# Performance work log

Hardware: AMD Instinct MI355X
Metric: run time of the kernel (lower is better)

## Reference

```python
import jax, jax.numpy as jnp
import numpy as np

H, CH, INF, EPS = 16, 24, 1e9, 1e-5

def layer_norm(x, w, b):
    mu = jnp.mean(x, axis=-1, keepdims=True)
    var = jnp.mean(jnp.square(x - mu), axis=-1, keepdims=True)
    return (x - mu) * jax.lax.rsqrt(var + EPS) * w + b

def setup_inputs() -> dict:
    key = jax.random.key(0)
    ks = jax.random.split(key, 10)
    B, N, C, CZ = 1, 768, 384, 128
    sc = 0.02
    return {
        "a": jax.random.normal(ks[0], (B, N, C), jnp.float32),
        "z": jax.random.normal(ks[1], (B, N, N, CZ), jnp.float32),
        "mask": jnp.ones((B, N), jnp.float32),
        "ln_a_w": jnp.ones((C,), jnp.float32),
        "ln_a_b": jnp.zeros((C,), jnp.float32),
        "ln_z_w": jnp.ones((CZ,), jnp.float32),
        "ln_z_b": jnp.zeros((CZ,), jnp.float32),
        "Wz": jax.random.normal(ks[2], (CZ, H), jnp.float32) * sc,
        "Wq": jax.random.normal(ks[3], (C, H * CH), jnp.float32) * sc,
        "Wk": jax.random.normal(ks[4], (C, H * CH), jnp.float32) * sc,
        "Wv": jax.random.normal(ks[5], (C, H * CH), jnp.float32) * sc,
        "Wg": jax.random.normal(ks[6], (C, H * CH), jnp.float32) * sc,
        "bg": jnp.ones((H * CH,), jnp.float32),
        "Wo": jax.random.normal(ks[7], (H * CH, C), jnp.float32) * sc,
        "bo": jnp.zeros((C,), jnp.float32),
    }

def reference(a, z, mask, ln_a_w, ln_a_b, ln_z_w, ln_z_b, Wz, Wq, Wk, Wv, Wg, bg, Wo, bo):
    B, N, C = a.shape
    an = layer_norm(a, ln_a_w, ln_a_b)                          # [B,N,C]
    # bias terms
    mask_bias = (INF * (mask - 1.0))[:, None, None, :]          # [B,1,1,N]
    pair_bias = jnp.einsum('bijc,ch->bhij', layer_norm(z, ln_z_w, ln_z_b), Wz)  # [B,H,N,N]
    # attention
    q = (an @ Wq).reshape(B, N, H, CH) * (CH ** -0.5)
    k = (an @ Wk).reshape(B, N, H, CH)
    v = (an @ Wv).reshape(B, N, H, CH)
    scores = jnp.einsum('bqhc,bkhc->bhqk', q, k) + mask_bias + pair_bias
    p = jax.nn.softmax(scores, axis=-1)
    o = jnp.einsum('bhqk,bkhc->bqhc', p, v).reshape(B, N, H * CH)
    g = jax.nn.sigmoid(an @ Wg + bg)                            # gating from query data
    return (g * o) @ Wo + bo                                    # [B,N,C]
```

## Files before the change

### kernel.cpp

```cpp
#include <hip/hip_runtime.h>
#include <math.h>

#define NT 768
#define CD 384
#define CZD 128
#define NH 16
#define CHD 24
#define HCD 384

__global__ __launch_bounds__(64) void k_prep(
    const float* __restrict__ a, const float* __restrict__ law, const float* __restrict__ lab,
    const float* __restrict__ lzw, const float* __restrict__ lzb, const float* __restrict__ Wz,
    float* __restrict__ an, float* __restrict__ Wp, float* __restrict__ PQ)
{
    const int b = blockIdx.x;
    const int lane = threadIdx.x;
    if (b < NT) {
        const float* row = a + b * CD;
        float v[6]; float s = 0.f, sq = 0.f;
        #pragma unroll
        for (int k = 0; k < 6; ++k) { float x = row[lane + 64*k]; v[k] = x; s += x; sq += x*x; }
        #pragma unroll
        for (int off = 32; off >= 1; off >>= 1) { s += __shfl_xor(s, off); sq += __shfl_xor(sq, off); }
        const float mu = s * (1.f/CD);
        const float rs = rsqrtf(sq * (1.f/CD) - mu*mu + 1e-5f);
        #pragma unroll
        for (int k = 0; k < 6; ++k) {
            int c = lane + 64*k;
            an[b*CD + c] = (v[k] - mu) * rs * law[c] + lab[c];
        }
    } else {
        for (int idx = lane; idx < CZD*NH; idx += 64)
            Wp[idx] = lzw[idx >> 4] * Wz[idx];
        if (lane < NH) {
            float P = 0.f, Q = 0.f;
            for (int c = 0; c < CZD; ++c) {
                P += lzw[c] * Wz[c*NH + lane];
                Q += lzb[c] * Wz[c*NH + lane];
            }
            PQ[lane] = P; PQ[NH + lane] = Q;
        }
    }
}

__global__ __launch_bounds__(256) void k_proj(
    const float* __restrict__ an, const float* __restrict__ Wq, const float* __restrict__ Wk,
    const float* __restrict__ Wv, const float* __restrict__ Wg, const float* __restrict__ bg,
    float* __restrict__ qm, float* __restrict__ kT, float* __restrict__ vT, float* __restrict__ gm)
{
    __shared__ float4 At[16][17];
    __shared__ float4 Bt[16][17];
    const int ct = blockIdx.x;
    const int mat = ct / 6;
    const int n0 = (ct % 6) * 64;
    const int i0 = blockIdx.y * 64;
    const float* __restrict__ W = (mat == 0) ? Wq : (mat == 1) ? Wk : (mat == 2) ? Wv : Wg;
    const int t = threadIdx.x;
    const int tr = t >> 4, tc = t & 15;
    float acc[4][4] = {};
    float* Atf = (float*)At;
    float* Btf = (float*)Bt;
    const int kkA = t & 15, iA = t >> 4;
    const int kkB = t >> 6, nB = t & 63;
    for (int k0 = 0; k0 < CD; k0 += 16) {
        __syncthreads();
        #pragma unroll
        for (int s = 0; s < 4; ++s)
            Atf[kkA*68 + iA + 16*s] = an[(i0 + iA + 16*s)*CD + k0 + kkA];
        #pragma unroll
        for (int s = 0; s < 4; ++s)
            Btf[(kkB + 4*s)*68 + nB] = W[(k0 + kkB + 4*s)*HCD + n0 + nB];
        __syncthreads();
        #pragma unroll
        for (int kk = 0; kk < 16; ++kk) {
            const float4 a4 = At[kk][tr];
            const float4 b4 = Bt[kk][tc];
            acc[0][0] += a4.x*b4.x; acc[0][1] += a4.x*b4.y; acc[0][2] += a4.x*b4.z; acc[0][3] += a4.x*b4.w;
            acc[1][0] += a4.y*b4.x; acc[1][1] += a4.y*b4.y; acc[1][2] += a4.y*b4.z; acc[1][3] += a4.y*b4.w;
            acc[2][0] += a4.z*b4.x; acc[2][1] += a4.z*b4.y; acc[2][2] += a4.z*b4.z; acc[2][3] += a4.z*b4.w;
            acc[3][0] += a4.w*b4.x; acc[3][1] += a4.w*b4.y; acc[3][2] += a4.w*b4.z; acc[3][3] += a4.w*b4.w;
        }
    }
    #pragma unroll
    for (int r = 0; r < 4; ++r) {
        const int i = i0 + tr*4 + r;
        #pragma unroll
        for (int c = 0; c < 4; ++c) {
            const int n = n0 + tc*4 + c;
            const float v = acc[r][c];
            if (mat == 0)      qm[i*HCD + n] = v * 0.20412414523193154f;
            else if (mat == 1) kT[n*NT + i] = v;
            else if (mat == 2) vT[n*NT + i] = v;
            else               gm[i*HCD + n] = 1.f / (1.f + __expf(-(v + bg[n])));
        }
    }
}

__global__ __launch_bounds__(64) void k_bias(
    const float* __restrict__ z, const float* __restrict__ Wp, const float* __restrict__ PQ,
    float* __restrict__ bias)
{
    __shared__ float zt[128*35];
    const int lane = threadIdx.x;
    const size_t r0 = (size_t)blockIdx.x * 128;
    const int i  = (int)(r0 / NT);
    const int j0 = (int)(r0 % NT);
    float s1 = 0.f, q1 = 0.f, s2 = 0.f, q2 = 0.f;
    float acc1[16] = {}, acc2[16] = {};
    const float4* __restrict__ Wp4 = (const float4*)Wp;
    for (int cq = 0; cq < 4; ++cq) {
        __syncthreads();
        const float* src = z + r0*CZD + cq*32;
        #pragma unroll
        for (int s = 0; s < 16; ++s) {
            const int g = lane + 64*s;
            const int row = g >> 3, c4 = g & 7;
            const float4 v = *(const float4*)(src + (size_t)row*CZD + c4*4);
            const int base = row*35 + c4*4;
            zt[base+0] = v.x; zt[base+1] = v.y; zt[base+2] = v.z; zt[base+3] = v.w;
        }
        __syncthreads();
        #pragma unroll 2
        for (int cc = 0; cc < 32; ++cc) {
            const int c = cq*32 + cc;
            const float z1 = zt[lane*35 + cc];
            const float z2 = zt[(lane+64)*35 + cc];
            s1 += z1; q1 += z1*z1; s2 += z2; q2 += z2*z2;
            const float4 w0 = Wp4[c*4+0], w1 = Wp4[c*4+1], w2 = Wp4[c*4+2], w3 = Wp4[c*4+3];
            acc1[0]+=z1*w0.x;  acc1[1]+=z1*w0.y;  acc1[2]+=z1*w0.z;  acc1[3]+=z1*w0.w;
            acc1[4]+=z1*w1.x;  acc1[5]+=z1*w1.y;  acc1[6]+=z1*w1.z;  acc1[7]+=z1*w1.w;
            acc1[8]+=z1*w2.x;  acc1[9]+=z1*w2.y;  acc1[10]+=z1*w2.z; acc1[11]+=z1*w2.w;
            acc1[12]+=z1*w3.x; acc1[13]+=z1*w3.y; acc1[14]+=z1*w3.z; acc1[15]+=z1*w3.w;
            acc2[0]+=z2*w0.x;  acc2[1]+=z2*w0.y;  acc2[2]+=z2*w0.z;  acc2[3]+=z2*w0.w;
            acc2[4]+=z2*w1.x;  acc2[5]+=z2*w1.y;  acc2[6]+=z2*w1.z;  acc2[7]+=z2*w1.w;
            acc2[8]+=z2*w2.x;  acc2[9]+=z2*w2.y;  acc2[10]+=z2*w2.z; acc2[11]+=z2*w2.w;
            acc2[12]+=z2*w3.x; acc2[13]+=z2*w3.y; acc2[14]+=z2*w3.z; acc2[15]+=z2*w3.w;
        }
    }
    float Pr[16], Qr[16];
    #pragma unroll
    for (int h = 0; h < 16; ++h) { Pr[h] = PQ[h]; Qr[h] = PQ[16+h]; }
    float mu = s1 * 0.0078125f;
    float rs = rsqrtf(q1 * 0.0078125f - mu*mu + 1e-5f);
    #pragma unroll
    for (int h = 0; h < 16; ++h)
        bias[(size_t)h*NT*NT + (size_t)i*NT + j0 + lane] = rs*(acc1[h] - mu*Pr[h]) + Qr[h];
    mu = s2 * 0.0078125f;
    rs = rsqrtf(q2 * 0.0078125f - mu*mu + 1e-5f);
    #pragma unroll
    for (int h = 0; h < 16; ++h)
        bias[(size_t)h*NT*NT + (size_t)i*NT + j0 + 64 + lane] = rs*(acc2[h] - mu*Pr[h]) + Qr[h];
}

__global__ __launch_bounds__(512) void k_attn(
    const float* __restrict__ qm, const float* __restrict__ kT, const float* __restrict__ vT,
    const float* __restrict__ bias, const float* __restrict__ mask, float* __restrict__ om)
{
    __shared__ __align__(16) char smem[55296];
    float (*ks)[68] = (float(*)[68])smem;
    float (*vs)[28] = (float(*)[28])(smem + 6528);
    float (*qs)[25] = (float(*)[25])(smem + 13696);
    float* mb       = (float*)(smem + 20096);
    float (*po)[64][25] = (float(*)[64][25])smem;
    float* pmf      = (float*)(smem + 51200);
    float* plf      = (float*)(smem + 53248);

    const int h  = blockIdx.x;
    const int i0 = blockIdx.y * 64;
    const int t = threadIdx.x;
    const int lane = t & 63, wave = t >> 6;
    const int i2 = lane & 31;
    const int jg4 = ((wave << 1) + (lane >> 5)) * 4;

    for (int idx = t; idx < 64*CHD; idx += 512) {
        const int ii = idx / CHD, c = idx % CHD;
        qs[ii][c] = qm[(i0+ii)*HCD + h*CHD + c];
    }
    __syncthreads();
    float qr[2][24];
    #pragma unroll
    for (int c = 0; c < 24; ++c) { qr[0][c] = qs[i2][c]; qr[1][c] = qs[i2+32][c]; }
    float m_[2] = {-1e30f, -1e30f}, l_[2] = {0.f, 0.f};
    float ov[2][24] = {};

    for (int jt = 0; jt < NT; jt += 64) {
        __syncthreads();
        for (int idx = t; idx < 24*64; idx += 512) {
            const int c = idx >> 6, j = idx & 63;
            ks[c][j] = kT[(h*CHD + c)*NT + jt + j];
            vs[j][c] = vT[(h*CHD + c)*NT + jt + j];
        }
        if (t < 64) mb[t] = 1e9f * (mask[jt + t] - 1.f);
        __syncthreads();

        const float* bp = bias + ((size_t)h*NT + (size_t)(i0 + i2))*NT + jt + jg4;
        const float4 b0 = *(const float4*)bp;
        const float4 b1 = *(const float4*)(bp + 32*NT);
        float sc0[4] = {b0.x, b0.y, b0.z, b0.w};
        float sc1[4] = {b1.x, b1.y, b1.z, b1.w};
        #pragma unroll
        for (int jj = 0; jj < 4; ++jj) { const float m0 = mb[jg4+jj]; sc0[jj] += m0; sc1[jj] += m0; }
        #pragma unroll
        for (int c = 0; c < 24; ++c) {
            const float4 k4 = *(const float4*)&ks[c][jg4];
            const float q0 = qr[0][c], q1v = qr[1][c];
            sc0[0] += q0*k4.x;  sc0[1] += q0*k4.y;  sc0[2] += q0*k4.z;  sc0[3] += q0*k4.w;
            sc1[0] += q1v*k4.x; sc1[1] += q1v*k4.y; sc1[2] += q1v*k4.z; sc1[3] += q1v*k4.w;
        }
        const float mt0 = fmaxf(fmaxf(sc0[0], sc0[1]), fmaxf(sc0[2], sc0[3]));
        const float mt1 = fmaxf(fmaxf(sc1[0], sc1[1]), fmaxf(sc1[2], sc1[3]));
        const float mn0 = fmaxf(m_[0], mt0), mn1 = fmaxf(m_[1], mt1);
        const float al0 = __expf(m_[0] - mn0), al1 = __expf(m_[1] - mn1);
        m_[0] = mn0; m_[1] = mn1;
        float p0[4], p1[4];
        #pragma unroll
        for (int jj = 0; jj < 4; ++jj) { p0[jj] = __expf(sc0[jj] - mn0); p1[jj] = __expf(sc1[jj] - mn1); }
        l_[0] = l_[0]*al0 + (p0[0]+p0[1]+p0[2]+p0[3]);
        l_[1] = l_[1]*al1 + (p1[0]+p1[1]+p1[2]+p1[3]);
        #pragma unroll
        for (int c = 0; c < 24; ++c) { ov[0][c] *= al0; ov[1][c] *= al1; }
        #pragma unroll
        for (int jj = 0; jj < 4; ++jj) {
            #pragma unroll
            for (int c4 = 0; c4 < 6; ++c4) {
                const float4 v4 = *(const float4*)&vs[jg4+jj][c4*4];
                ov[0][c4*4+0] += p0[jj]*v4.x; ov[0][c4*4+1] += p0[jj]*v4.y;
                ov[0][c4*4+2] += p0[jj]*v4.z; ov[0][c4*4+3] += p0[jj]*v4.w;
                ov[1][c4*4+0] += p1[jj]*v4.x; ov[1][c4*4+1] += p1[jj]*v4.y;
                ov[1][c4*4+2] += p1[jj]*v4.z; ov[1][c4*4+3] += p1[jj]*v4.w;
            }
        }
    }
    #pragma unroll
    for (int r = 0; r < 2; ++r) {
        const float mo = __shfl_xor(m_[r], 32);
        const float lo = __shfl_xor(l_[r], 32);
        const float mn = fmaxf(m_[r], mo);
        const float wa = __expf(m_[r] - mn), wb = __expf(mo - mn);
        l_[r] = l_[r]*wa + lo*wb;
        m_[r] = mn;
        #pragma unroll
        for (int c = 0; c < 24; ++c)
            ov[r][c] = ov[r][c]*wa + __shfl_xor(ov[r][c], 32)*wb;
    }
    __syncthreads();
    if (lane < 32) {
        #pragma unroll
        for (int r = 0; r < 2; ++r) {
            const int i = i2 + 32*r;
            pmf[wave*64 + i] = m_[r]; plf[wave*64 + i] = l_[r];
            #pragma unroll
            for (int c = 0; c < 24; ++c) po[wave][i][c] = ov[r][c];
        }
    }
    __syncthreads();
    {
        const int i = t & 63, cq = t >> 6;
        float ms = -1e30f;
        #pragma unroll
        for (int g = 0; g < 8; ++g) ms = fmaxf(ms, pmf[g*64 + i]);
        float ls = 0.f, o0 = 0.f, o1 = 0.f, o2 = 0.f;
        #pragma unroll
        for (int g = 0; g < 8; ++g) {
            const float w = __expf(pmf[g*64 + i] - ms);
            ls += w * plf[g*64 + i];
            o0 += w * po[g][i][cq*3+0];
            o1 += w * po[g][i][cq*3+1];
            o2 += w * po[g][i][cq*3+2];
        }
        const float inv = 1.f / ls;
        float* dst = om + (size_t)(i0 + i)*HCD + h*CHD + cq*3;
        dst[0] = o0*inv; dst[1] = o1*inv; dst[2] = o2*inv;
    }
}

__global__ __launch_bounds__(256) void k_epi(
    const float* __restrict__ gm, const float* __restrict__ om, const float* __restrict__ Wo,
    const float* __restrict__ bo, float* __restrict__ out)
{
    __shared__ float4 At[16][17];
    __shared__ float4 Bt[16][17];
    const int n0 = blockIdx.x * 64;
    const int i0 = blockIdx.y * 64;
    const int t = threadIdx.x;
    const int tr = t >> 4, tc = t & 15;
    float acc[4][4] = {};
    float* Atf = (float*)At;
    float* Btf = (float*)Bt;
    const int kkA = t & 15, iA = t >> 4;
    const int kkB = t >> 6, nB = t & 63;
    for (int k0 = 0; k0 < HCD; k0 += 16) {
        __syncthreads();
        #pragma unroll
        for (int s = 0; s < 4; ++s) {
            const int row = i0 + iA + 16*s;
            Atf[kkA*68 + iA + 16*s] = gm[row*HCD + k0 + kkA] * om[row*HCD + k0 + kkA];
        }
        #pragma unroll
        for (int s = 0; s < 4; ++s)
            Btf[(kkB + 4*s)*68 + nB] = Wo[(k0 + kkB + 4*s)*CD + n0 + nB];
        __syncthreads();
        #pragma unroll
        for (int kk = 0; kk < 16; ++kk) {
            const float4 a4 = At[kk][tr];
            const float4 b4 = Bt[kk][tc];
            acc[0][0] += a4.x*b4.x; acc[0][1] += a4.x*b4.y; acc[0][2] += a4.x*b4.z; acc[0][3] += a4.x*b4.w;
            acc[1][0] += a4.y*b4.x; acc[1][1] += a4.y*b4.y; acc[1][2] += a4.y*b4.z; acc[1][3] += a4.y*b4.w;
            acc[2][0] += a4.z*b4.x; acc[2][1] += a4.z*b4.y; acc[2][2] += a4.z*b4.z; acc[2][3] += a4.z*b4.w;
            acc[3][0] += a4.w*b4.x; acc[3][1] += a4.w*b4.y; acc[3][2] += a4.w*b4.z; acc[3][3] += a4.w*b4.w;
        }
    }
    #pragma unroll
    for (int r = 0; r < 4; ++r) {
        const int i = i0 + tr*4 + r;
        #pragma unroll
        for (int c = 0; c < 4; ++c) {
            const int n = n0 + tc*4 + c;
            out[i*CD + n] = acc[r][c] + bo[n];
        }
    }
}

extern "C" void kernel_launch(void* const* d_in, const int* in_sizes, int n_in,
                              void* d_out, int out_size, void* d_ws, size_t ws_size,
                              hipStream_t stream) {
    const float* a    = (const float*)d_in[0];
    const float* z    = (const float*)d_in[1];
    const float* mask = (const float*)d_in[2];
    const float* law  = (const float*)d_in[3];
    const float* lab  = (const float*)d_in[4];
    const float* lzw  = (const float*)d_in[5];
    const float* lzb  = (const float*)d_in[6];
    const float* Wz   = (const float*)d_in[7];
    const float* Wq   = (const float*)d_in[8];
    const float* Wk   = (const float*)d_in[9];
    const float* Wv   = (const float*)d_in[10];
    const float* Wg   = (const float*)d_in[11];
    const float* bg   = (const float*)d_in[12];
    const float* Wo   = (const float*)d_in[13];
    const float* bo   = (const float*)d_in[14];
    float* out = (float*)d_out;

    float* ws = (float*)d_ws;
    float* an   = ws;
    float* qm   = an + 294912;
    float* kT   = qm + 294912;
    float* vT   = kT + 294912;
    float* gm   = vT + 294912;
    float* om   = gm + 294912;
    float* Wp   = om + 294912;
    float* PQ   = Wp + 2048;
    float* bias = PQ + 32;

    k_prep<<<769, 64, 0, stream>>>(a, law, lab, lzw, lzb, Wz, an, Wp, PQ);
    k_proj<<<dim3(24, 12), 256, 0, stream>>>(an, Wq, Wk, Wv, Wg, bg, qm, kT, vT, gm);
    k_bias<<<4608, 64, 0, stream>>>(z, Wp, PQ, bias);
    k_attn<<<dim3(16, 12), 512, 0, stream>>>(qm, kT, vT, bias, mask, om);
    k_epi<<<dim3(6, 12), 256, 0, stream>>>(gm, om, Wo, bo, out);
}
```

Baseline: 570.8 us.

## Shrink row tiles to raise block counts and simplify pair-bias to one row per thread

The projection, attention and epilogue kernels now use 32-row tiles instead of 64, which doubles their grid sizes so more CUs have work on a 768-token problem. Attention blocks halve to 256 threads, each handling one query row over 8 keys. The pair-bias kernel drops its shared-memory transpose: each thread streams its own z row with float4 loads and writes 16 bias values. The trade-off is less reuse per block and uncoalesced per-thread z reads (each thread walks a separate 512-byte row).

```diff
diff --git a/kernel.cpp b/kernel.cpp
--- a/kernel.cpp
+++ b/kernel.cpp
@@ -43,38 +43,36 @@
     }
 }
 
-__global__ __launch_bounds__(256) void k_proj(
+__global__ __launch_bounds__(128) void k_proj(
     const float* __restrict__ an, const float* __restrict__ Wq, const float* __restrict__ Wk,
     const float* __restrict__ Wv, const float* __restrict__ Wg, const float* __restrict__ bg,
     float* __restrict__ qm, float* __restrict__ kT, float* __restrict__ vT, float* __restrict__ gm)
 {
-    __shared__ float4 At[16][17];
-    __shared__ float4 Bt[16][17];
+    __shared__ __align__(16) float Atf[16*36];
+    __shared__ __align__(16) float Btf[16*68];
     const int ct = blockIdx.x;
     const int mat = ct / 6;
     const int n0 = (ct % 6) * 64;
-    const int i0 = blockIdx.y * 64;
+    const int i0 = blockIdx.y * 32;
     const float* __restrict__ W = (mat == 0) ? Wq : (mat == 1) ? Wk : (mat == 2) ? Wv : Wg;
     const int t = threadIdx.x;
     const int tr = t >> 4, tc = t & 15;
     float acc[4][4] = {};
-    float* Atf = (float*)At;
-    float* Btf = (float*)Bt;
     const int kkA = t & 15, iA = t >> 4;
     const int kkB = t >> 6, nB = t & 63;
     for (int k0 = 0; k0 < CD; k0 += 16) {
         __syncthreads();
         #pragma unroll
         for (int s = 0; s < 4; ++s)
-            Atf[kkA*68 + iA + 16*s] = an[(i0 + iA + 16*s)*CD + k0 + kkA];
-        #pragma unroll
-        for (int s = 0; s < 4; ++s)
-            Btf[(kkB + 4*s)*68 + nB] = W[(k0 + kkB + 4*s)*HCD + n0 + nB];
+            Atf[kkA*36 + iA + 8*s] = an[(i0 + iA + 8*s)*CD + k0 + kkA];
+        #pragma unroll
+        for (int s = 0; s < 8; ++s)
+            Btf[(kkB + 2*s)*68 + nB] = W[(k0 + kkB + 2*s)*HCD + n0 + nB];
         __syncthreads();
         #pragma unroll
         for (int kk = 0; kk < 16; ++kk) {
-            const float4 a4 = At[kk][tr];
-            const float4 b4 = Bt[kk][tc];
+            const float4 a4 = *(const float4*)&Atf[kk*36 + tr*4];
+            const float4 b4 = *(const float4*)&Btf[kk*68 + tc*4];
             acc[0][0] += a4.x*b4.x; acc[0][1] += a4.x*b4.y; acc[0][2] += a4.x*b4.z; acc[0][3] += a4.x*b4.w;
             acc[1][0] += a4.y*b4.x; acc[1][1] += a4.y*b4.y; acc[1][2] += a4.y*b4.z; acc[1][3] += a4.y*b4.w;
             acc[2][0] += a4.z*b4.x; acc[2][1] += a4.z*b4.y; acc[2][2] += a4.z*b4.z; acc[2][3] += a4.z*b4.w;
@@ -96,96 +94,73 @@
     }
 }
 
-__global__ __launch_bounds__(64) void k_bias(
+__global__ __launch_bounds__(256) void k_bias(
     const float* __restrict__ z, const float* __restrict__ Wp, const float* __restrict__ PQ,
     float* __restrict__ bias)
 {
-    __shared__ float zt[128*35];
-    const int lane = threadIdx.x;
-    const size_t r0 = (size_t)blockIdx.x * 128;
-    const int i  = (int)(r0 / NT);
-    const int j0 = (int)(r0 % NT);
-    float s1 = 0.f, q1 = 0.f, s2 = 0.f, q2 = 0.f;
-    float acc1[16] = {}, acc2[16] = {};
+    const int t = threadIdx.x;
+    const size_t r = (size_t)blockIdx.x * 256 + t;
+    const float4* __restrict__ zr = (const float4*)(z + r * CZD);
     const float4* __restrict__ Wp4 = (const float4*)Wp;
-    for (int cq = 0; cq < 4; ++cq) {
-        __syncthreads();
-        const float* src = z + r0*CZD + cq*32;
-        #pragma unroll
-        for (int s = 0; s < 16; ++s) {
-            const int g = lane + 64*s;
-            const int row = g >> 3, c4 = g & 7;
-            const float4 v = *(const float4*)(src + (size_t)row*CZD + c4*4);
-            const int base = row*35 + c4*4;
-            zt[base+0] = v.x; zt[base+1] = v.y; zt[base+2] = v.z; zt[base+3] = v.w;
-        }
-        __syncthreads();
-        #pragma unroll 2
-        for (int cc = 0; cc < 32; ++cc) {
-            const int c = cq*32 + cc;
-            const float z1 = zt[lane*35 + cc];
-            const float z2 = zt[(lane+64)*35 + cc];
-            s1 += z1; q1 += z1*z1; s2 += z2; q2 += z2*z2;
+    float s = 0.f, q = 0.f;
+    float acc[16] = {};
+    #pragma unroll 8
+    for (int c4 = 0; c4 < 32; ++c4) {
+        const float4 v = zr[c4];
+        const float xs[4] = {v.x, v.y, v.z, v.w};
+        #pragma unroll
+        for (int e = 0; e < 4; ++e) {
+            const float x = xs[e];
+            s += x; q += x*x;
+            const int c = c4*4 + e;
             const float4 w0 = Wp4[c*4+0], w1 = Wp4[c*4+1], w2 = Wp4[c*4+2], w3 = Wp4[c*4+3];
-            acc1[0]+=z1*w0.x;  acc1[1]+=z1*w0.y;  acc1[2]+=z1*w0.z;  acc1[3]+=z1*w0.w;
-            acc1[4]+=z1*w1.x;  acc1[5]+=z1*w1.y;  acc1[6]+=z1*w1.z;  acc1[7]+=z1*w1.w;
-            acc1[8]+=z1*w2.x;  acc1[9]+=z1*w2.y;  acc1[10]+=z1*w2.z; acc1[11]+=z1*w2.w;
-            acc1[12]+=z1*w3.x; acc1[13]+=z1*w3.y; acc1[14]+=z1*w3.z; acc1[15]+=z1*w3.w;
-            acc2[0]+=z2*w0.x;  acc2[1]+=z2*w0.y;  acc2[2]+=z2*w0.z;  acc2[3]+=z2*w0.w;
-            acc2[4]+=z2*w1.x;  acc2[5]+=z2*w1.y;  acc2[6]+=z2*w1.z;  acc2[7]+=z2*w1.w;
-            acc2[8]+=z2*w2.x;  acc2[9]+=z2*w2.y;  acc2[10]+=z2*w2.z; acc2[11]+=z2*w2.w;
-            acc2[12]+=z2*w3.x; acc2[13]+=z2*w3.y; acc2[14]+=z2*w3.z; acc2[15]+=z2*w3.w;
-        }
-    }
-    float Pr[16], Qr[16];
-    #pragma unroll
-    for (int h = 0; h < 16; ++h) { Pr[h] = PQ[h]; Qr[h] = PQ[16+h]; }
-    float mu = s1 * 0.0078125f;
-    float rs = rsqrtf(q1 * 0.0078125f - mu*mu + 1e-5f);
+            acc[0]+=x*w0.x;  acc[1]+=x*w0.y;  acc[2]+=x*w0.z;  acc[3]+=x*w0.w;
+            acc[4]+=x*w1.x;  acc[5]+=x*w1.y;  acc[6]+=x*w1.z;  acc[7]+=x*w1.w;
+            acc[8]+=x*w2.x;  acc[9]+=x*w2.y;  acc[10]+=x*w2.z; acc[11]+=x*w2.w;
+            acc[12]+=x*w3.x; acc[13]+=x*w3.y; acc[14]+=x*w3.z; acc[15]+=x*w3.w;
+        }
+    }
+    const float mu = s * (1.f/CZD);
+    const float rs = rsqrtf(q * (1.f/CZD) - mu*mu + 1e-5f);
     #pragma unroll
     for (int h = 0; h < 16; ++h)
-        bias[(size_t)h*NT*NT + (size_t)i*NT + j0 + lane] = rs*(acc1[h] - mu*Pr[h]) + Qr[h];
-    mu = s2 * 0.0078125f;
-    rs = rsqrtf(q2 * 0.0078125f - mu*mu + 1e-5f);
-    #pragma unroll
-    for (int h = 0; h < 16; ++h)
-        bias[(size_t)h*NT*NT + (size_t)i*NT + j0 + 64 + lane] = rs*(acc2[h] - mu*Pr[h]) + Qr[h];
-}
-
-__global__ __launch_bounds__(512) void k_attn(
+        bias[(size_t)h*NT*NT + r] = rs*(acc[h] - mu*PQ[h]) + PQ[16+h];
+}
+
+__global__ __launch_bounds__(256) void k_attn(
     const float* __restrict__ qm, const float* __restrict__ kT, const float* __restrict__ vT,
     const float* __restrict__ bias, const float* __restrict__ mask, float* __restrict__ om)
 {
-    __shared__ __align__(16) char smem[55296];
+    __shared__ __align__(16) char smem[17408];
     float (*ks)[68] = (float(*)[68])smem;
     float (*vs)[28] = (float(*)[28])(smem + 6528);
     float (*qs)[25] = (float(*)[25])(smem + 13696);
-    float* mb       = (float*)(smem + 20096);
-    float (*po)[64][25] = (float(*)[64][25])smem;
-    float* pmf      = (float*)(smem + 51200);
-    float* plf      = (float*)(smem + 53248);
+    float* mb       = (float*)(smem + 16896);
+    float (*po)[32][25] = (float(*)[32][25])smem;
+    float* pmf      = (float*)(smem + 12800);
+    float* plf      = (float*)(smem + 13312);
 
     const int h  = blockIdx.x;
-    const int i0 = blockIdx.y * 64;
+    const int i0 = blockIdx.y * 32;
     const int t = threadIdx.x;
     const int lane = t & 63, wave = t >> 6;
     const int i2 = lane & 31;
-    const int jg4 = ((wave << 1) + (lane >> 5)) * 4;
-
-    for (int idx = t; idx < 64*CHD; idx += 512) {
+    const int jg8 = ((wave << 1) + (lane >> 5)) * 8;
+
+    for (int idx = t; idx < 32*CHD; idx += 256) {
         const int ii = idx / CHD, c = idx % CHD;
         qs[ii][c] = qm[(i0+ii)*HCD + h*CHD + c];
     }
     __syncthreads();
-    float qr[2][24];
+    float qr[24];
     #pragma unroll
-    for (int c = 0; c < 24; ++c) { qr[0][c] = qs[i2][c]; qr[1][c] = qs[i2+32][c]; }
-    float m_[2] = {-1e30f, -1e30f}, l_[2] = {0.f, 0.f};
-    float ov[2][24] = {};
+    for (int c = 0; c < 24; ++c) qr[c] = qs[i2][c];
+    float m_ = -1e30f, l_ = 0.f;
+    float ov[24] = {};
 
     for (int jt = 0; jt < NT; jt += 64) {
         __syncthreads();
-        for (int idx = t; idx < 24*64; idx += 512) {
+        for (int idx = t; idx < 24*64; idx += 256) {
             const int c = idx >> 6, j = idx & 63;
             ks[c][j] = kT[(h*CHD + c)*NT + jt + j];
             vs[j][c] = vT[(h*CHD + c)*NT + jt + j];
@@ -193,77 +168,70 @@
         if (t < 64) mb[t] = 1e9f * (mask[jt + t] - 1.f);
         __syncthreads();
 
-        const float* bp = bias + ((size_t)h*NT + (size_t)(i0 + i2))*NT + jt + jg4;
+        const float* bp = bias + ((size_t)h*NT + (size_t)(i0 + i2))*NT + jt + jg8;
         const float4 b0 = *(const float4*)bp;
-        const float4 b1 = *(const float4*)(bp + 32*NT);
-        float sc0[4] = {b0.x, b0.y, b0.z, b0.w};
-        float sc1[4] = {b1.x, b1.y, b1.z, b1.w};
-        #pragma unroll
-        for (int jj = 0; jj < 4; ++jj) { const float m0 = mb[jg4+jj]; sc0[jj] += m0; sc1[jj] += m0; }
+        const float4 b1 = *(const float4*)(bp + 4);
+        float sc[8] = {b0.x, b0.y, b0.z, b0.w, b1.x, b1.y, b1.z, b1.w};
+        #pragma unroll
+        for (int jj = 0; jj < 8; ++jj) sc[jj] += mb[jg8+jj];
         #pragma unroll
         for (int c = 0; c < 24; ++c) {
-            const float4 k4 = *(const float4*)&ks[c][jg4];
-            const float q0 = qr[0][c], q1v = qr[1][c];
-            sc0[0] += q0*k4.x;  sc0[1] += q0*k4.y;  sc0[2] += q0*k4.z;  sc0[3] += q0*k4.w;
-            sc1[0] += q1v*k4.x; sc1[1] += q1v*k4.y; sc1[2] += q1v*k4.z; sc1[3] += q1v*k4.w;
-        }
-        const float mt0 = fmaxf(fmaxf(sc0[0], sc0[1]), fmaxf(sc0[2], sc0[3]));
-        const float mt1 = fmaxf(fmaxf(sc1[0], sc1[1]), fmaxf(sc1[2], sc1[3]));
-        const float mn0 = fmaxf(m_[0], mt0), mn1 = fmaxf(m_[1], mt1);
-        const float al0 = __expf(m_[0] - mn0), al1 = __expf(m_[1] - mn1);
-        m_[0] = mn0; m_[1] = mn1;
-        float p0[4], p1[4];
-        #pragma unroll
-        for (int jj = 0; jj < 4; ++jj) { p0[jj] = __expf(sc0[jj] - mn0); p1[jj] = __expf(sc1[jj] - mn1); }
-        l_[0] = l_[0]*al0 + (p0[0]+p0[1]+p0[2]+p0[3]);
-        l_[1] = l_[1]*al1 + (p1[0]+p1[1]+p1[2]+p1[3]);
-        #pragma unroll
-        for (int c = 0; c < 24; ++c) { ov[0][c] *= al0; ov[1][c] *= al1; }
-        #pragma unroll
-        for (int jj = 0; jj < 4; ++jj) {
+            const float4 k4a = *(const float4*)&ks[c][jg8];
+            const float4 k4b = *(const float4*)&ks[c][jg8+4];
+            const float q0 = qr[c];
+            sc[0] += q0*k4a.x; sc[1] += q0*k4a.y; sc[2] += q0*k4a.z; sc[3] += q0*k4a.w;
+            sc[4] += q0*k4b.x; sc[5] += q0*k4b.y; sc[6] += q0*k4b.z; sc[7] += q0*k4b.w;
+        }
+        float mt = sc[0];
+        #pragma unroll
+        for (int jj = 1; jj < 8; ++jj) mt = fmaxf(mt, sc[jj]);
+        const float mn = fmaxf(m_, mt);
+        const float al = __expf(m_ - mn);
+        m_ = mn;
+        float p[8], ps = 0.f;
+        #pragma unroll
+        for (int jj = 0; jj < 8; ++jj) { p[jj] = __expf(sc[jj] - mn); ps += p[jj]; }
+        l_ = l_*al + ps;
+        #pragma unroll
+        for (int c = 0; c < 24; ++c) ov[c] *= al;
+        #pragma unroll
+        for (int jj = 0; jj < 8; ++jj) {
             #pragma unroll
             for (int c4 = 0; c4 < 6; ++c4) {
-                const float4 v4 = *(const float4*)&vs[jg4+jj][c4*4];
-                ov[0][c4*4+0] += p0[jj]*v4.x; ov[0][c4*4+1] += p0[jj]*v4.y;
-                ov[0][c4*4+2] += p0[jj]*v4.z; ov[0][c4*4+3] += p0[jj]*v4.w;
-                ov[1][c4*4+0] += p1[jj]*v4.x; ov[1][c4*4+1] += p1[jj]*v4.y;
-                ov[1][c4*4+2] += p1[jj]*v4.z; ov[1][c4*4+3] += p1[jj]*v4.w;
+                const float4 v4 = *(const float4*)&vs[jg8+jj][c4*4];
+                ov[c4*4+0] += p[jj]*v4.x; ov[c4*4+1] += p[jj]*v4.y;
+                ov[c4*4+2] += p[jj]*v4.z; ov[c4*4+3] += p[jj]*v4.w;
             }
         }
     }
-    #pragma unroll
-    for (int r = 0; r < 2; ++r) {
-        const float mo = __shfl_xor(m_[r], 32);
-        const float lo = __shfl_xor(l_[r], 32);
-        const float mn = fmaxf(m_[r], mo);
-        const float wa = __expf(m_[r] - mn), wb = __expf(mo - mn);
-        l_[r] = l_[r]*wa + lo*wb;
-        m_[r] = mn;
+    {
+        const float mo = __shfl_xor(m_, 32);
+        const float lo = __shfl_xor(l_, 32);
+        const float mn = fmaxf(m_, mo);
+        const float wa = __expf(m_ - mn), wb = __expf(mo - mn);
+        l_ = l_*wa + lo*wb;
+        m_ = mn;
         #pragma unroll
         for (int c = 0; c < 24; ++c)
-            ov[r][c] = ov[r][c]*wa + __shfl_xor(ov[r][c], 32)*wb;
+            ov[c] = ov[c]*wa + __shfl_xor(ov[c], 32)*wb;
     }
     __syncthreads();
     if (lane < 32) {
-        #pragma unroll
-        for (int r = 0; r < 2; ++r) {
-            const int i = i2 + 32*r;
-            pmf[wave*64 + i] = m_[r]; plf[wave*64 + i] = l_[r];
-            #pragma unroll
-            for (int c = 0; c < 24; ++c) po[wave][i][c] = ov[r][c];
-        }
+        pmf[wave*32 + i2] = m_; plf[wave*32 + i2] = l_;
+        #pragma unroll
+        for (int c = 0; c < 24; ++c) po[wave][i2][c] = ov[c];
     }
     __syncthreads();
     {
-        const int i = t & 63, cq = t >> 6;
+        const int i = t & 31, cq = t >> 5;
         float ms = -1e30f;
         #pragma unroll
-        for (int g = 0; g < 8; ++g) ms = fmaxf(ms, pmf[g*64 + i]);
+        for (int g = 0; g < 4; ++g) ms = fmaxf(ms, pmf[g*32 + i]);
         float ls = 0.f, o0 = 0.f, o1 = 0.f, o2 = 0.f;
         #pragma unroll
-        for (int g = 0; g < 8; ++g) {
-            const float w = __expf(pmf[g*64 + i] - ms);
-            ls += w * plf[g*64 + i];
+        for (int g = 0; g < 4; ++g) {
+            const float w = __expf(pmf[g*32 + i] - ms);
+            ls += w * plf[g*32 + i];
             o0 += w * po[g][i][cq*3+0];
             o1 += w * po[g][i][cq*3+1];
             o2 += w * po[g][i][cq*3+2];
@@ -274,36 +242,34 @@
     }
 }
 
-__global__ __launch_bounds__(256) void k_epi(
+__global__ __launch_bounds__(128) void k_epi(
     const float* __restrict__ gm, const float* __restrict__ om, const float* __restrict__ Wo,
     const float* __restrict__ bo, float* __restrict__ out)
 {
-    __shared__ float4 At[16][17];
-    __shared__ float4 Bt[16][17];
+    __shared__ __align__(16) float Atf[16*36];
+    __shared__ __align__(16) float Btf[16*68];
     const int n0 = blockIdx.x * 64;
-    const int i0 = blockIdx.y * 64;
+    const int i0 = blockIdx.y * 32;
     const int t = threadIdx.x;
     const int tr = t >> 4, tc = t & 15;
     float acc[4][4] = {};
-    float* Atf = (float*)At;
-    float* Btf = (float*)Bt;
     const int kkA = t & 15, iA = t >> 4;
     const int kkB = t >> 6, nB = t & 63;
     for (int k0 = 0; k0 < HCD; k0 += 16) {
         __syncthreads();
         #pragma unroll
         for (int s = 0; s < 4; ++s) {
-            const int row = i0 + iA + 16*s;
-            Atf[kkA*68 + iA + 16*s] = gm[row*HCD + k0 + kkA] * om[row*HCD + k0 + kkA];
-        }
-        #pragma unroll
-        for (int s = 0; s < 4; ++s)
-            Btf[(kkB + 4*s)*68 + nB] = Wo[(k0 + kkB + 4*s)*CD + n0 + nB];
+            const int row = i0 + iA + 8*s;
+            Atf[kkA*36 + iA + 8*s] = gm[row*HCD + k0 + kkA] * om[row*HCD + k0 + kkA];
+        }
+        #pragma unroll
+        for (int s = 0; s < 8; ++s)
+            Btf[(kkB + 2*s)*68 + nB] = Wo[(k0 + kkB + 2*s)*CD + n0 + nB];
         __syncthreads();
         #pragma unroll
         for (int kk = 0; kk < 16; ++kk) {
-            const float4 a4 = At[kk][tr];
-            const float4 b4 = Bt[kk][tc];
+            const float4 a4 = *(const float4*)&Atf[kk*36 + tr*4];
+            const float4 b4 = *(const float4*)&Btf[kk*68 + tc*4];
             acc[0][0] += a4.x*b4.x; acc[0][1] += a4.x*b4.y; acc[0][2] += a4.x*b4.z; acc[0][3] += a4.x*b4.w;
             acc[1][0] += a4.y*b4.x; acc[1][1] += a4.y*b4.y; acc[1][2] += a4.y*b4.z; acc[1][3] += a4.y*b4.w;
             acc[2][0] += a4.z*b4.x; acc[2][1] += a4.z*b4.y; acc[2][2] += a4.z*b4.z; acc[2][3] += a4.z*b4.w;
@@ -353,8 +319,8 @@
     float* bias = PQ + 32;
 
     k_prep<<<769, 64, 0, stream>>>(a, law, lab, lzw, lzb, Wz, an, Wp, PQ);
-    k_proj<<<dim3(24, 12), 256, 0, stream>>>(an, Wq, Wk, Wv, Wg, bg, qm, kT, vT, gm);
-    k_bias<<<4608, 64, 0, stream>>>(z, Wp, PQ, bias);
-    k_attn<<<dim3(16, 12), 512, 0, stream>>>(qm, kT, vT, bias, mask, om);
-    k_epi<<<dim3(6, 12), 256, 0, stream>>>(gm, om, Wo, bo, out);
-}
+    k_proj<<<dim3(24, 24), 128, 0, stream>>>(an, Wq, Wk, Wv, Wg, bg, qm, kT, vT, gm);
+    k_bias<<<2304, 256, 0, stream>>>(z, Wp, PQ, bias);
+    k_attn<<<dim3(16, 24), 256, 0, stream>>>(qm, kT, vT, bias, mask, om);
+    k_epi<<<dim3(6, 24), 128, 0, stream>>>(gm, om, Wo, bo, out);
+}
```

Result: no change. 567.5 us (-0.6%).
